# Performance work log

Hardware: AMD Instinct MI355X
Metric: run time of the kernel (lower is better)

The kernel has to match this reference:

```python
import jax, jax.numpy as jnp
import numpy as np

EPS = 1e-6

def _complex_linear(xr, xi, wr, wi):
    # torch Linear: y = x @ W.T ; complex: (xr+i*xi)(Wr+i*Wi)
    yr = jnp.einsum('bsd,ed->bse', xr, wr) - jnp.einsum('bsd,ed->bse', xi, wi)
    yi = jnp.einsum('bsd,ed->bse', xr, wi) + jnp.einsum('bsd,ed->bse', xi, wr)
    return yr, yi

def setup_inputs() -> dict:
    key = jax.random.key(0)
    ks = jax.random.split(key, 12)
    B, S, D = 32768, 16, 64
    inp = {
        'z_real': jax.random.normal(ks[0], (B, D), jnp.float32),
        'z_imag': jax.random.normal(ks[1], (B, D), jnp.float32),
        'mem':    jax.random.normal(ks[2], (B, S, 2 * D), jnp.float32),
        'ptr':    jax.random.uniform(ks[3], (B, S), jnp.float32),
        'ctrl':   jax.random.normal(ks[4], (B, 3), jnp.float32),
        'wq_r': jax.random.normal(ks[5], (D, D), jnp.float32) / np.sqrt(D),
        'wq_i': jax.random.normal(ks[6], (D, D), jnp.float32) / np.sqrt(D),
        'wk_r': jax.random.normal(ks[7], (D, D), jnp.float32) / np.sqrt(D),
        'wk_i': jax.random.normal(ks[8], (D, D), jnp.float32) / np.sqrt(D),
        'wv_r': jax.random.normal(ks[9], (D, D), jnp.float32) / np.sqrt(D),
        'wv_i': jax.random.normal(ks[10], (D, D), jnp.float32) / np.sqrt(D),
    }
    return inp

def reference(z_real, z_imag, mem, ptr, ctrl, wq_r, wq_i, wk_r, wk_i, wv_r, wv_i):
    D = z_real.shape[-1]
    # soft push/pop/stay gates, normalized
    g = jax.nn.sigmoid(ctrl)  # (B,3)
    push, pop, stay = g[:, 0:1], g[:, 1:2], g[:, 2:3]
    total = push + pop + stay + EPS
    push, pop, stay = push / total, pop / total, stay / total
    # pointer update via rolls
    ptr_up = jnp.roll(ptr, 1, axis=1)
    ptr_down = jnp.roll(ptr, -1, axis=1)
    new_ptr = push * ptr_up + pop * ptr_down + stay * ptr  # (B,S)
    # memory write
    z_flat = jnp.concatenate([z_real, z_imag], axis=-1)  # (B,2D)
    mem_new = mem * (1.0 - push[..., None]) + push[..., None] * z_flat[:, None, :]
    mr, mi = mem_new[..., :D], mem_new[..., D:]  # (B,S,D) complex memory
    # complex attention over stack slots
    qr, qi = _complex_linear(mr, mi, wq_r, wq_i)
    kr, ki = _complex_linear(mr, mi, wk_r, wk_i)
    vr, vi = _complex_linear(mr, mi, wv_r, wv_i)
    q_flat = jnp.concatenate([qr, qi], axis=-1)  # (B,S,2D)
    k_flat = jnp.concatenate([kr, ki], axis=-1)
    scale = D ** (-0.5)
    scores = jnp.einsum('bse,bte->bst', q_flat, k_flat) * scale  # (B,S,S)
    attn = jax.nn.softmax(scores, axis=-1)
    ar = jnp.einsum('bst,btd->bsd', attn, vr)
    ai = jnp.einsum('bst,btd->bsd', attn, vi)
    att_flat = jnp.concatenate([ar, ai], axis=-1)  # (B,S,2D)
    # pointer-weighted read
    read_flat = (att_flat * new_ptr[..., None]).sum(axis=1)  # (B,2D)
    z_read_r, z_read_i = read_flat[:, :D], read_flat[:, D:]
    active_slots = (new_ptr > 0.1).astype(jnp.float32).sum(axis=1).mean()
    return (z_read_r, z_read_i, mem_new, new_ptr, active_slots)
```

## Files before the change

kernel.cpp:

```cpp
#include <hip/hip_runtime.h>


typedef __bf16 bf16x8 __attribute__((ext_vector_type(8)));
typedef float  f32x4  __attribute__((ext_vector_type(4)));
typedef float  f4     __attribute__((ext_vector_type(4)));

#define B_TOT   32768
#define GRID_WG 512
#define NWAVES  4096
#define BPW     8
#define LOG2E   1.4426950408889634f
#define EXSC    0.18033688011112042f

__device__ __forceinline__ unsigned short f2bf(float x) {
  __bf16 h = (__bf16)x;
  return __builtin_bit_cast(unsigned short, h);
}
__device__ __forceinline__ float rcp_f(float x) { return __builtin_amdgcn_rcpf(x); }
__device__ __forceinline__ float ex2_f(float x) { return __builtin_amdgcn_exp2f(x); }
__device__ __forceinline__ float sigm(float x) { return rcp_f(1.0f + ex2_f(-LOG2E * x)); }

__global__ void ems_fin(const unsigned int* __restrict__ c, float* __restrict__ out) {
  if (threadIdx.x == 0) out[0] = (float)(*c) * (1.0f / 32768.0f);
}

__global__ void __launch_bounds__(128)
ems_mt(const float* __restrict__ wqr, const float* __restrict__ wqi,
       const float* __restrict__ wkr, const float* __restrict__ wki,
       unsigned short* __restrict__ mt, unsigned int* __restrict__ cnt)
{
  if (blockIdx.x == 0 && threadIdx.x == 0) *cnt = 0u;
  __shared__ float sK[128];
  const int e2 = (int)blockIdx.x;
  const int e  = (int)threadIdx.x;
  float kv;
  if (e < 64) kv = (e2 < 64) ? wkr[e*64 + e2]      : -wki[e*64 + (e2-64)];
  else        kv = (e2 < 64) ? wki[(e-64)*64 + e2] :  wkr[(e-64)*64 + (e2-64)];
  sK[e] = kv;
  __syncthreads();
  float acc = 0.0f;
  #pragma unroll 8
  for (int Ep = 0; Ep < 64; ++Ep) {
    float q = (e < 64) ? wqr[Ep*64 + e] : -wqi[Ep*64 + (e-64)];
    acc += q * sK[Ep];
  }
  #pragma unroll 8
  for (int Ep = 0; Ep < 64; ++Ep) {
    float q = (e < 64) ? wqi[Ep*64 + e] : wqr[Ep*64 + (e-64)];
    acc += q * sK[64 + Ep];
  }
  mt[e2*128 + e] = f2bf(acc);
}

__global__ void __launch_bounds__(512, 4)
ems_main(const float* __restrict__ z_real, const float* __restrict__ z_imag,
         const float* __restrict__ mem,    const float* __restrict__ ptrv,
         const float* __restrict__ ctrl,
         const float* __restrict__ wvr,    const float* __restrict__ wvi,
         const unsigned short* __restrict__ mt,
         float* __restrict__ out_zr, float* __restrict__ out_zi,
         float* __restrict__ out_mem, float* __restrict__ out_ptr,
         unsigned int* __restrict__ ws_cnt)
{
  __shared__ __align__(16) unsigned short lds[40960];

  const int tid = (int)threadIdx.x;

  for (int idx = tid; idx < 16384; idx += 512) {
    int e2 = idx >> 7, e = idx & 127;
    lds[(e2 << 7) + (((e >> 3) ^ (e2 & 15)) << 3) + (e & 7)] = mt[idx];
  }
  #pragma unroll
  for (int m = 0; m < 2; ++m) {
    const float* wp = m ? wvi : wvr;
    for (int idx = tid; idx < 4096; idx += 512) {
      int e = idx >> 6, d = idx & 63;
      lds[16384 + (m << 12) + (e << 6) + (((d >> 3) ^ (e & 7)) << 3) + (d & 7)] = f2bf(wp[idx]);
    }
  }
  __syncthreads();

  const int lane = tid & 63;
  const int wv   = tid >> 6;
  const int c    = lane & 15;
  const int g    = lane >> 4;

  unsigned short* SY = &lds[24576 + (wv << 11)];

  const f4* mem4 = (const f4*)mem;
  const f4* zr4  = (const f4*)z_real;
  const f4* zi4  = (const f4*)z_imag;
  f4* omem4 = (f4*)out_mem;

  unsigned int active_acc = 0u;
  const int b0 = (int)blockIdx.x * 8 + wv;

  for (int it = 0; it < BPW; ++it) {
    const int b = b0 + it * NWAVES;

    f4 cm[8], cz[8];
    #pragma unroll
    for (int t4 = 0; t4 < 4; ++t4) {
      int i4 = b*512 + c*32 + t4*8 + g*2;
      cm[2*t4]   = mem4[i4];
      cm[2*t4+1] = mem4[i4+1];
    }
    {
      int zb = b*16 + g*2;
      cz[0] = zr4[zb];   cz[1] = zr4[zb+1];
      cz[2] = zr4[zb+8]; cz[3] = zr4[zb+9];
      cz[4] = zi4[zb];   cz[5] = zi4[zb+1];
      cz[6] = zi4[zb+8]; cz[7] = zi4[zb+9];
    }

    float pu = sigm(ctrl[b*3+0]);
    float po = sigm(ctrl[b*3+1]);
    float st = sigm(ctrl[b*3+2]);
    float rt = rcp_f(pu + po + st + 1e-6f);
    pu *= rt; po *= rt; st *= rt;

    float pm = ptrv[b*16 + ((c+15)&15)];
    float pp = ptrv[b*16 + ((c+ 1)&15)];
    float pc = ptrv[b*16 + c];
    float np = pu*pm + po*pp + st*pc;
    if (g == 0) out_ptr[b*16 + c] = np;
    unsigned long long ball = __ballot(np > 0.1f);
    active_acc += (unsigned int)__popcll(ball & 0xFFFFull);

    float om = 1.0f - pu;
    bf16x8 af[4], afn[2];
    #pragma unroll
    for (int t4 = 0; t4 < 4; ++t4) {
      f4 r0 = cm[2*t4]   * om + pu * cz[2*t4];
      f4 r1 = cm[2*t4+1] * om + pu * cz[2*t4+1];
      int i4 = b*512 + c*32 + t4*8 + g*2;
      omem4[i4]   = r0;
      omem4[i4+1] = r1;
      #pragma unroll
      for (int k = 0; k < 4; ++k) {
        af[t4][k]   = (__bf16)r0[k];
        af[t4][4+k] = (__bf16)r1[k];
      }
      if (t4 >= 2) {
        #pragma unroll
        for (int k = 0; k < 4; ++k) {
          afn[t4-2][k]   = (__bf16)(-r0[k]);
          afn[t4-2][4+k] = (__bf16)(-r1[k]);
        }
      }
    }

    #pragma unroll
    for (int n2 = 0; n2 < 8; ++n2) {
      int e2 = (n2 << 4) + c;
      f32x4 acc = {0.f,0.f,0.f,0.f};
      #pragma unroll
      for (int T = 0; T < 4; ++T) {
        bf16x8 am = *(const bf16x8*)&lds[(e2 << 7) + ((((T << 2) + g) ^ c) << 3)];
        acc = __builtin_amdgcn_mfma_f32_16x16x32_bf16(am, af[T], acc, 0, 0, 0);
      }
      uint2 pk;
      pk.x = (unsigned)f2bf(acc[0]) | ((unsigned)f2bf(acc[1]) << 16);
      pk.y = (unsigned)f2bf(acc[2]) | ((unsigned)f2bf(acc[3]) << 16);
      *(uint2*)&SY[(c << 7) + ((((n2 << 1) + (g >> 1)) ^ c) << 3) + ((g & 1) << 2)] = pk;
    }

    f32x4 sc = {0.f,0.f,0.f,0.f};
    #pragma unroll
    for (int T = 0; T < 4; ++T) {
      bf16x8 yb = *(const bf16x8*)&SY[(c << 7) + ((((T << 2) + g) ^ c) << 3)];
      sc = __builtin_amdgcn_mfma_f32_16x16x32_bf16(af[T], yb, sc, 0, 0, 0);
    }

    float e0 = ex2_f(sc[0] * EXSC);
    float e1 = ex2_f(sc[1] * EXSC);
    float e2v = ex2_f(sc[2] * EXSC);
    float e3 = ex2_f(sc[3] * EXSC);
    float r = (e0 + e1) + (e2v + e3);
    r += __shfl_xor(r, 16, 64);
    r += __shfl_xor(r, 32, 64);
    float u = np * rcp_f(r);
    float v0 = u*e0, v1 = u*e1, v2 = u*e2v, v3 = u*e3;
    #pragma unroll
    for (int d = 1; d <= 8; d <<= 1) {
      v0 += __shfl_xor(v0, d, 64);
      v1 += __shfl_xor(v1, d, 64);
      v2 += __shfl_xor(v2, d, 64);
      v3 += __shfl_xor(v3, d, 64);
    }
    float w4[4] = { v0, v1, v2, v3 };

    #pragma unroll
    for (int n = 0; n < 4; ++n) {
      int eb = 16384 + (((n << 4) + c) << 6);
      int e7 = c & 7;
      f32x4 ar = {0.f,0.f,0.f,0.f}, ai = {0.f,0.f,0.f,0.f};
      #pragma unroll
      for (int t = 0; t < 2; ++t) {
        int ch = (((t << 2) + g) ^ e7) << 3;
        bf16x8 fr = *(const bf16x8*)&lds[eb + ch];
        bf16x8 fi = *(const bf16x8*)&lds[eb + 4096 + ch];
        ar = __builtin_amdgcn_mfma_f32_16x16x32_bf16(af[t],   fr, ar, 0,0,0);
        ai = __builtin_amdgcn_mfma_f32_16x16x32_bf16(af[t],   fi, ai, 0,0,0);
        ar = __builtin_amdgcn_mfma_f32_16x16x32_bf16(afn[t],  fi, ar, 0,0,0);
        ai = __builtin_amdgcn_mfma_f32_16x16x32_bf16(af[t+2], fr, ai, 0,0,0);
      }
      float prr = ar[0]*w4[0] + ar[1]*w4[1] + ar[2]*w4[2] + ar[3]*w4[3];
      float pri = ai[0]*w4[0] + ai[1]*w4[1] + ai[2]*w4[2] + ai[3]*w4[3];
      prr += __shfl_xor(prr, 16, 64);
      prr += __shfl_xor(prr, 32, 64);
      pri += __shfl_xor(pri, 16, 64);
      pri += __shfl_xor(pri, 32, 64);
      if (g == 0) out_zr[b*64 + (n << 4) + c] = prr;
      if (g == 1) out_zi[b*64 + (n << 4) + c] = pri;
    }
  }

  __syncthreads();
  unsigned int* cnt_lds = (unsigned int*)&lds[24576];
  if (tid == 0) *cnt_lds = 0u;
  __syncthreads();
  if (lane == 0) atomicAdd(cnt_lds, active_acc);
  __syncthreads();
  if (tid == 0) atomicAdd(ws_cnt, *cnt_lds);
}

extern "C" void kernel_launch(void* const* d_in, const int* in_sizes, int n_in,
                              void* d_out, int out_size, void* d_ws, size_t ws_size,
                              hipStream_t stream) {
  const float* z_real = (const float*)d_in[0];
  const float* z_imag = (const float*)d_in[1];
  const float* memp   = (const float*)d_in[2];
  const float* ptrv   = (const float*)d_in[3];
  const float* ctrl   = (const float*)d_in[4];
  const float* wq_r   = (const float*)d_in[5];
  const float* wq_i   = (const float*)d_in[6];
  const float* wk_r   = (const float*)d_in[7];
  const float* wk_i   = (const float*)d_in[8];
  const float* wv_r   = (const float*)d_in[9];
  const float* wv_i   = (const float*)d_in[10];

  float* out     = (float*)d_out;
  float* out_zr  = out;
  float* out_zi  = out + 2097152;
  float* out_mem = out + 4194304;
  float* out_ptr = out + 71303168;
  float* out_sc  = out + 71827456;

  unsigned int*   cnt = (unsigned int*)d_ws;
  unsigned short* mtp = (unsigned short*)((char*)d_ws + 1024);

  ems_mt<<<128, 128, 0, stream>>>(wq_r, wq_i, wk_r, wk_i, mtp, cnt);
  ems_main<<<GRID_WG, 512, 0, stream>>>(z_real, z_imag, memp, ptrv, ctrl,
                                        wv_r, wv_i, mtp,
                                        out_zr, out_zi, out_mem, out_ptr, cnt);
  ems_fin<<<1, 64, 0, stream>>>(cnt, out_sc);
}
```

Before: 150.7 us.

## Prepack weight fragments in MFMA layout and read them from global instead of LDS

The precomputed Q·K^T matrix and the V weights are now stored in workspace already arranged as per-lane MFMA fragments, with a new small kernel that converts and packs the V weights. The main kernel loads these fragments straight from global memory (expecting L1/L2 hits) instead of staging them in LDS at block start. This removes the per-block LDS fill and barrier and shrinks LDS use, and the occupancy hint rises from 4 to 6. The cost is repeated global/cache loads inside the per-batch loop and one extra kernel launch.

```diff
diff --git a/kernel.cpp b/kernel.cpp
--- a/kernel.cpp
+++ b/kernel.cpp
@@ -27,7 +27,7 @@
 __global__ void __launch_bounds__(128)
 ems_mt(const float* __restrict__ wqr, const float* __restrict__ wqi,
        const float* __restrict__ wkr, const float* __restrict__ wki,
-       unsigned short* __restrict__ mt, unsigned int* __restrict__ cnt)
+       unsigned short* __restrict__ mtf, unsigned int* __restrict__ cnt)
 {
   if (blockIdx.x == 0 && threadIdx.x == 0) *cnt = 0u;
   __shared__ float sK[128];
@@ -49,48 +49,53 @@
     float q = (e < 64) ? wqi[Ep*64 + e] : wqr[Ep*64 + (e-64)];
     acc += q * sK[64 + Ep];
   }
-  mt[e2*128 + e] = f2bf(acc);
-}
-
-__global__ void __launch_bounds__(512, 4)
+  int n2 = e2 >> 4, c = e2 & 15;
+  int T  = e >> 5, g = (e >> 3) & 3, j = e & 7;
+  mtf[(((n2*4 + T)*64) + 16*g + c)*8 + j] = f2bf(acc);
+}
+
+__global__ void __launch_bounds__(512)
+ems_wv(const float* __restrict__ wvr, const float* __restrict__ wvi,
+       unsigned short* __restrict__ wvf_r, unsigned short* __restrict__ wvf_i)
+{
+  int idx = (int)blockIdx.x * 512 + (int)threadIdx.x;
+  int e = idx >> 6, d = idx & 63;
+  int n = e >> 4, c = e & 15;
+  int t = d >> 5, g = (d >> 3) & 3, j = d & 7;
+  int dst = (((n*2 + t)*64) + 16*g + c)*8 + j;
+  wvf_r[dst] = f2bf(wvr[idx]);
+  wvf_i[dst] = f2bf(wvi[idx]);
+}
+
+__global__ void __launch_bounds__(512, 6)
 ems_main(const float* __restrict__ z_real, const float* __restrict__ z_imag,
          const float* __restrict__ mem,    const float* __restrict__ ptrv,
          const float* __restrict__ ctrl,
-         const float* __restrict__ wvr,    const float* __restrict__ wvi,
-         const unsigned short* __restrict__ mt,
+         const unsigned short* __restrict__ mtf,
+         const unsigned short* __restrict__ wvf_r,
+         const unsigned short* __restrict__ wvf_i,
          float* __restrict__ out_zr, float* __restrict__ out_zi,
          float* __restrict__ out_mem, float* __restrict__ out_ptr,
          unsigned int* __restrict__ ws_cnt)
 {
-  __shared__ __align__(16) unsigned short lds[40960];
-
-  const int tid = (int)threadIdx.x;
-
-  for (int idx = tid; idx < 16384; idx += 512) {
-    int e2 = idx >> 7, e = idx & 127;
-    lds[(e2 << 7) + (((e >> 3) ^ (e2 & 15)) << 3) + (e & 7)] = mt[idx];
-  }
-  #pragma unroll
-  for (int m = 0; m < 2; ++m) {
-    const float* wp = m ? wvi : wvr;
-    for (int idx = tid; idx < 4096; idx += 512) {
-      int e = idx >> 6, d = idx & 63;
-      lds[16384 + (m << 12) + (e << 6) + (((d >> 3) ^ (e & 7)) << 3) + (d & 7)] = f2bf(wp[idx]);
-    }
-  }
-  __syncthreads();
-
+  __shared__ __align__(16) unsigned short lds[8 * 2048];
+
+  const int tid  = (int)threadIdx.x;
   const int lane = tid & 63;
   const int wv   = tid >> 6;
   const int c    = lane & 15;
   const int g    = lane >> 4;
 
-  unsigned short* SY = &lds[24576 + (wv << 11)];
+  unsigned short* SY = &lds[wv << 11];
 
   const f4* mem4 = (const f4*)mem;
   const f4* zr4  = (const f4*)z_real;
   const f4* zi4  = (const f4*)z_imag;
   f4* omem4 = (f4*)out_mem;
+
+  const uint4* mt4 = (const uint4*)mtf;
+  const uint4* wr4 = (const uint4*)wvf_r;
+  const uint4* wi4 = (const uint4*)wvf_i;
 
   unsigned int active_acc = 0u;
   const int b0 = (int)blockIdx.x * 8 + wv;
@@ -152,11 +157,10 @@
 
     #pragma unroll
     for (int n2 = 0; n2 < 8; ++n2) {
-      int e2 = (n2 << 4) + c;
       f32x4 acc = {0.f,0.f,0.f,0.f};
       #pragma unroll
       for (int T = 0; T < 4; ++T) {
-        bf16x8 am = *(const bf16x8*)&lds[(e2 << 7) + ((((T << 2) + g) ^ c) << 3)];
+        bf16x8 am = __builtin_bit_cast(bf16x8, mt4[(((n2 << 2) + T) << 6) + lane]);
         acc = __builtin_amdgcn_mfma_f32_16x16x32_bf16(am, af[T], acc, 0, 0, 0);
       }
       uint2 pk;
@@ -192,14 +196,12 @@
 
     #pragma unroll
     for (int n = 0; n < 4; ++n) {
-      int eb = 16384 + (((n << 4) + c) << 6);
-      int e7 = c & 7;
       f32x4 ar = {0.f,0.f,0.f,0.f}, ai = {0.f,0.f,0.f,0.f};
       #pragma unroll
       for (int t = 0; t < 2; ++t) {
-        int ch = (((t << 2) + g) ^ e7) << 3;
-        bf16x8 fr = *(const bf16x8*)&lds[eb + ch];
-        bf16x8 fi = *(const bf16x8*)&lds[eb + 4096 + ch];
+        int fi4 = (((n << 1) + t) << 6) + lane;
+        bf16x8 fr = __builtin_bit_cast(bf16x8, wr4[fi4]);
+        bf16x8 fi = __builtin_bit_cast(bf16x8, wi4[fi4]);
         ar = __builtin_amdgcn_mfma_f32_16x16x32_bf16(af[t],   fr, ar, 0,0,0);
         ai = __builtin_amdgcn_mfma_f32_16x16x32_bf16(af[t],   fi, ai, 0,0,0);
         ar = __builtin_amdgcn_mfma_f32_16x16x32_bf16(afn[t],  fi, ar, 0,0,0);
@@ -217,7 +219,7 @@
   }
 
   __syncthreads();
-  unsigned int* cnt_lds = (unsigned int*)&lds[24576];
+  unsigned int* cnt_lds = (unsigned int*)&lds[0];
   if (tid == 0) *cnt_lds = 0u;
   __syncthreads();
   if (lane == 0) atomicAdd(cnt_lds, active_acc);
@@ -247,12 +249,15 @@
   float* out_ptr = out + 71303168;
   float* out_sc  = out + 71827456;
 
-  unsigned int*   cnt = (unsigned int*)d_ws;
-  unsigned short* mtp = (unsigned short*)((char*)d_ws + 1024);
-
-  ems_mt<<<128, 128, 0, stream>>>(wq_r, wq_i, wk_r, wk_i, mtp, cnt);
+  unsigned int*   cnt   = (unsigned int*)d_ws;
+  unsigned short* mtf   = (unsigned short*)((char*)d_ws + 1024);
+  unsigned short* wvf_r = (unsigned short*)((char*)d_ws + 33792);
+  unsigned short* wvf_i = (unsigned short*)((char*)d_ws + 33792 + 8192);
+
+  ems_mt<<<128, 128, 0, stream>>>(wq_r, wq_i, wk_r, wk_i, mtf, cnt);
+  ems_wv<<<8, 512, 0, stream>>>(wv_r, wv_i, wvf_r, wvf_i);
   ems_main<<<GRID_WG, 512, 0, stream>>>(z_real, z_imag, memp, ptrv, ctrl,
-                                        wv_r, wv_i, mtp,
+                                        mtf, wvf_r, wvf_i,
                                         out_zr, out_zi, out_mem, out_ptr, cnt);
   ems_fin<<<1, 64, 0, stream>>>(cnt, out_sc);
 }
```

Result: slower. 489.2 us (+224.5%).

## Split gate/pointer computation into prep kernel and use DPP reductions

Applied to the files above, without the earlier changes.

Moves the sigmoid gating, pointer update, out_ptr write and active-slot counting into a separate lightweight prep kernel that writes a per-batch push gate to workspace. The main kernel then just loads the new pointer and push gate, drops its end-of-block LDS/atomic reduction, and uses an empty asm barrier to keep the mem/z loads issued early. The 16-lane weight reductions switch from shfl_xor to DPP row operations. The trade is an extra kernel launch plus an extra global round trip for the pointer and gate data in exchange for a shorter main kernel.

```diff
diff --git a/kernel.cpp b/kernel.cpp
--- a/kernel.cpp
+++ b/kernel.cpp
@@ -19,6 +19,19 @@
 __device__ __forceinline__ float rcp_f(float x) { return __builtin_amdgcn_rcpf(x); }
 __device__ __forceinline__ float ex2_f(float x) { return __builtin_amdgcn_exp2f(x); }
 __device__ __forceinline__ float sigm(float x) { return rcp_f(1.0f + ex2_f(-LOG2E * x)); }
+
+__device__ __forceinline__ float dpp_sum16(float v) {
+  int x;
+  x = __builtin_amdgcn_update_dpp(0, __builtin_bit_cast(int, v), 0xB1, 0xF, 0xF, false);
+  v += __builtin_bit_cast(float, x);
+  x = __builtin_amdgcn_update_dpp(0, __builtin_bit_cast(int, v), 0x4E, 0xF, 0xF, false);
+  v += __builtin_bit_cast(float, x);
+  x = __builtin_amdgcn_update_dpp(0, __builtin_bit_cast(int, v), 0x141, 0xF, 0xF, false);
+  v += __builtin_bit_cast(float, x);
+  x = __builtin_amdgcn_update_dpp(0, __builtin_bit_cast(int, v), 0x140, 0xF, 0xF, false);
+  v += __builtin_bit_cast(float, x);
+  return v;
+}
 
 __global__ void ems_fin(const unsigned int* __restrict__ c, float* __restrict__ out) {
   if (threadIdx.x == 0) out[0] = (float)(*c) * (1.0f / 32768.0f);
@@ -52,15 +65,42 @@
   mt[e2*128 + e] = f2bf(acc);
 }
 
+__global__ void __launch_bounds__(256)
+ems_prep(const float* __restrict__ ptrv, const float* __restrict__ ctrl,
+         float* __restrict__ out_ptr, float* __restrict__ pub,
+         unsigned int* __restrict__ cnt)
+{
+  __shared__ unsigned int c_lds;
+  if (threadIdx.x == 0) c_lds = 0u;
+  __syncthreads();
+  int idx = (int)blockIdx.x * 256 + (int)threadIdx.x;
+  int b = idx >> 4, s = idx & 15;
+  float pu = sigm(ctrl[b*3+0]);
+  float po = sigm(ctrl[b*3+1]);
+  float st = sigm(ctrl[b*3+2]);
+  float rt = rcp_f(pu + po + st + 1e-6f);
+  pu *= rt; po *= rt; st *= rt;
+  float pm = ptrv[b*16 + ((s+15)&15)];
+  float pp = ptrv[b*16 + ((s+ 1)&15)];
+  float pc = ptrv[b*16 + s];
+  float np = pu*pm + po*pp + st*pc;
+  out_ptr[idx] = np;
+  if (s == 0) pub[b] = pu;
+  unsigned long long ball = __ballot(np > 0.1f);
+  if ((threadIdx.x & 63) == 0) atomicAdd(&c_lds, (unsigned int)__popcll(ball));
+  __syncthreads();
+  if (threadIdx.x == 0) atomicAdd(cnt, c_lds);
+}
+
 __global__ void __launch_bounds__(512, 4)
 ems_main(const float* __restrict__ z_real, const float* __restrict__ z_imag,
-         const float* __restrict__ mem,    const float* __restrict__ ptrv,
-         const float* __restrict__ ctrl,
+         const float* __restrict__ mem,
+         const float* __restrict__ np_in,
+         const float* __restrict__ pub,
          const float* __restrict__ wvr,    const float* __restrict__ wvi,
          const unsigned short* __restrict__ mt,
          float* __restrict__ out_zr, float* __restrict__ out_zi,
-         float* __restrict__ out_mem, float* __restrict__ out_ptr,
-         unsigned int* __restrict__ ws_cnt)
+         float* __restrict__ out_mem)
 {
   __shared__ __align__(16) unsigned short lds[40960];
 
@@ -92,7 +132,6 @@
   const f4* zi4  = (const f4*)z_imag;
   f4* omem4 = (f4*)out_mem;
 
-  unsigned int active_acc = 0u;
   const int b0 = (int)blockIdx.x * 8 + wv;
 
   for (int it = 0; it < BPW; ++it) {
@@ -112,20 +151,12 @@
       cz[4] = zi4[zb];   cz[5] = zi4[zb+1];
       cz[6] = zi4[zb+8]; cz[7] = zi4[zb+9];
     }
-
-    float pu = sigm(ctrl[b*3+0]);
-    float po = sigm(ctrl[b*3+1]);
-    float st = sigm(ctrl[b*3+2]);
-    float rt = rcp_f(pu + po + st + 1e-6f);
-    pu *= rt; po *= rt; st *= rt;
-
-    float pm = ptrv[b*16 + ((c+15)&15)];
-    float pp = ptrv[b*16 + ((c+ 1)&15)];
-    float pc = ptrv[b*16 + c];
-    float np = pu*pm + po*pp + st*pc;
-    if (g == 0) out_ptr[b*16 + c] = np;
-    unsigned long long ball = __ballot(np > 0.1f);
-    active_acc += (unsigned int)__popcll(ball & 0xFFFFull);
+    float np = np_in[b*16 + c];
+    float pu = pub[b];
+    asm volatile("" : "+v"(cm[0]), "+v"(cm[1]), "+v"(cm[2]), "+v"(cm[3]),
+                      "+v"(cm[4]), "+v"(cm[5]), "+v"(cm[6]), "+v"(cm[7]),
+                      "+v"(cz[0]), "+v"(cz[1]), "+v"(cz[2]), "+v"(cz[3]),
+                      "+v"(cz[4]), "+v"(cz[5]), "+v"(cz[6]), "+v"(cz[7]));
 
     float om = 1.0f - pu;
     bf16x8 af[4], afn[2];
@@ -180,15 +211,11 @@
     r += __shfl_xor(r, 16, 64);
     r += __shfl_xor(r, 32, 64);
     float u = np * rcp_f(r);
-    float v0 = u*e0, v1 = u*e1, v2 = u*e2v, v3 = u*e3;
-    #pragma unroll
-    for (int d = 1; d <= 8; d <<= 1) {
-      v0 += __shfl_xor(v0, d, 64);
-      v1 += __shfl_xor(v1, d, 64);
-      v2 += __shfl_xor(v2, d, 64);
-      v3 += __shfl_xor(v3, d, 64);
-    }
-    float w4[4] = { v0, v1, v2, v3 };
+    float w4[4];
+    w4[0] = dpp_sum16(u * e0);
+    w4[1] = dpp_sum16(u * e1);
+    w4[2] = dpp_sum16(u * e2v);
+    w4[3] = dpp_sum16(u * e3);
 
     #pragma unroll
     for (int n = 0; n < 4; ++n) {
@@ -215,14 +242,6 @@
       if (g == 1) out_zi[b*64 + (n << 4) + c] = pri;
     }
   }
-
-  __syncthreads();
-  unsigned int* cnt_lds = (unsigned int*)&lds[24576];
-  if (tid == 0) *cnt_lds = 0u;
-  __syncthreads();
-  if (lane == 0) atomicAdd(cnt_lds, active_acc);
-  __syncthreads();
-  if (tid == 0) atomicAdd(ws_cnt, *cnt_lds);
 }
 
 extern "C" void kernel_launch(void* const* d_in, const int* in_sizes, int n_in,
@@ -249,10 +268,12 @@
 
   unsigned int*   cnt = (unsigned int*)d_ws;
   unsigned short* mtp = (unsigned short*)((char*)d_ws + 1024);
+  float*          pub = (float*)((char*)d_ws + 65536);
 
   ems_mt<<<128, 128, 0, stream>>>(wq_r, wq_i, wk_r, wk_i, mtp, cnt);
-  ems_main<<<GRID_WG, 512, 0, stream>>>(z_real, z_imag, memp, ptrv, ctrl,
-                                        wv_r, wv_i, mtp,
-                                        out_zr, out_zi, out_mem, out_ptr, cnt);
+  ems_prep<<<2048, 256, 0, stream>>>(ptrv, ctrl, out_ptr, pub, cnt);
+  ems_main<<<GRID_WG, 512, 0, stream>>>(z_real, z_imag, memp,
+                                        out_ptr, pub, wv_r, wv_i, mtp,
+                                        out_zr, out_zi, out_mem);
   ems_fin<<<1, 64, 0, stream>>>(cnt, out_sc);
 }
```

Result: slower. 174.9 us (+16.0%).
